# Performance work log

Hardware: AMD Instinct MI355X
Metric: run time of the kernel (lower is better)

Reference implementation:

```python
import jax, jax.numpy as jnp
import numpy as np

N = 100000   # nodes
E = 1600000  # edges
IN, H1, H2, OUT = 128, 256, 128, 16


def setup_inputs() -> dict:
    key = jax.random.key(0)
    ks = jax.random.split(key, 20)

    def lin(kw, fan_in, fan_out):
        s = 1.0 / np.sqrt(fan_in)
        return jax.random.uniform(kw, (fan_in, fan_out), jnp.float32, -s, s)

    inp = {
        "x": jax.random.normal(ks[0], (N, IN), jnp.float32),
        "edge_index": jax.random.randint(ks[1], (2, E), 0, N, jnp.int64),
        # main branch
        "W1": lin(ks[2], IN, H1), "b1": jnp.zeros((H1,), jnp.float32),
        "W2": lin(ks[3], H1, H2), "b2": jnp.zeros((H2,), jnp.float32),
        "Wc": lin(ks[4], H2, OUT), "bc": jnp.zeros((OUT,), jnp.float32),
        # encoder branch (4 GCN layers)
        "We1": lin(ks[5], IN, H2), "be1": jnp.zeros((H2,), jnp.float32),
        "We2": lin(ks[6], H2, H2), "be2": jnp.zeros((H2,), jnp.float32),
        "We3": lin(ks[7], H2, H2), "be3": jnp.zeros((H2,), jnp.float32),
        "We4": lin(ks[8], H2, H2), "be4": jnp.zeros((H2,), jnp.float32),
        # trustworthiness head
        "Wt": lin(ks[9], H2, 2), "bt": jnp.zeros((2,), jnp.float32),
    }
    return inp


def _gcn(x, W, b, row, col, dis):
    # PyG GCNConv: out = D^-1/2 (A + I) D^-1/2 (x W) + b
    xw = x @ W                                   # [N, F]
    norm = dis[row] * dis[col]                   # [E]
    msg = xw[row] * norm[:, None]                # [E, F]  (gather + scale)
    agg = jax.ops.segment_sum(msg, col, num_segments=N)
    agg = agg + xw * (dis * dis)[:, None]        # self-loop contribution
    return agg + b


def reference(x, edge_index, W1, b1, W2, b2, Wc, bc,
              We1, be1, We2, be2, We3, be3, We4, be4, Wt, bt):
    row, col = edge_index[0], edge_index[1]
    # degree with self-loops, shared across all conv layers (same graph)
    deg = jax.ops.segment_sum(jnp.ones((E,), x.dtype), col, num_segments=N) + 1.0
    dis = deg ** -0.5

    # classification branch
    h = jax.nn.relu(_gcn(x, W1, b1, row, col, dis))
    h = _gcn(h, W2, b2, row, col, dis)
    class_logits = h @ Wc + bc

    # encoder branch -> trust head
    h2 = _gcn(x, We1, be1, row, col, dis)
    h2 = _gcn(h2, We2, be2, row, col, dis)
    h2 = _gcn(h2, We3, be3, row, col, dis)
    h2 = _gcn(h2, We4, be4, row, col, dis)
    trust_prob = jax.nn.sigmoid(h2 @ Wt + bt)

    return (class_logits, trust_prob)
```

## Files before the change

### kernel.cpp

```cpp
#include <hip/hip_runtime.h>
#include <math.h>


#define SM_W2C   0
#define SM_T4    4096
#define SM_T3    4352
#define SM_T2    4608
#define SM_ME    4864
#define SM_CLSC  5120
#define SM_C1    5136
#define SM_C2    5138
#define SM_C3    5140
#define SM_FC    5142
#define SM_TOTAL 5248

typedef __attribute__((ext_vector_type(8))) short bf16x8;
typedef __attribute__((ext_vector_type(4))) float f32x4;
#define MFMA16(a, b, c) __builtin_amdgcn_mfma_f32_16x16x32_bf16(a, b, c, 0, 0, 0)

__device__ inline unsigned short f2bf(float f) {
  unsigned u = __float_as_uint(f);
  u += 0x7fffu + ((u >> 16) & 1u);
  return (unsigned short)(u >> 16);
}
__device__ inline float bf2f(unsigned short h) {
  return __uint_as_float((unsigned)h << 16);
}

__global__ __launch_bounds__(256) void k_deg(const int* __restrict__ ei,
                                             int* __restrict__ deg, int E, int N) {
  int e = blockIdx.x * 256 + threadIdx.x;
  if (e < E) {
    unsigned c = (unsigned)ei[E + e];
    if (c >= (unsigned)N) c = 0;
    atomicAdd(&deg[c], 1);
  }
}

__global__ __launch_bounds__(1024) void k_scan1(const int* __restrict__ deg,
                                                int* __restrict__ rowptr,
                                                int* __restrict__ bsum,
                                                float* __restrict__ dis,
                                                int* __restrict__ cnt, int n) {
  __shared__ int wsum[16];
  int tid = threadIdx.x, lane = tid & 63, wid = tid >> 6;
  int i = blockIdx.x * 1024 + tid;
  int v = (i < n) ? deg[i] : 0;
  if (i < n) {
    dis[i] = 1.0f / sqrtf((float)v + 1.0f);
    cnt[i] = 0;
  }
  int x = v;
  #pragma unroll
  for (int off = 1; off < 64; off <<= 1) {
    int t = __shfl_up(x, off, 64);
    if (lane >= off) x += t;
  }
  if (lane == 63) wsum[wid] = x;
  __syncthreads();
  if (wid == 0 && lane < 16) {
    int ws = wsum[lane];
    #pragma unroll
    for (int off = 1; off < 16; off <<= 1) {
      int t = __shfl_up(ws, off, 64);
      if (lane >= off) ws += t;
    }
    wsum[lane] = ws;
  }
  __syncthreads();
  int incl = x + (wid ? wsum[wid - 1] : 0);
  if (i < n) rowptr[i + 1] = incl;
  if (tid == 0) bsum[blockIdx.x] = wsum[15];
}

__global__ __launch_bounds__(128) void k_scan2(int* __restrict__ bsum,
                                               int* __restrict__ rowptr, int B) {
  __shared__ int s[128];
  int tid = threadIdx.x;
  s[tid] = (tid < B) ? bsum[tid] : 0;
  __syncthreads();
  if (tid == 0) {
    int acc = 0;
    for (int j = 0; j < B; ++j) { int t = s[j]; s[j] = acc; acc += t; }
    rowptr[0] = 0;
  }
  __syncthreads();
  if (tid < B) bsum[tid] = s[tid];
}

__global__ __launch_bounds__(256) void k_scan3(int* __restrict__ rowptr,
                                               const int* __restrict__ bsum, int n) {
  int i = blockIdx.x * 256 + threadIdx.x;
  if (i < n) rowptr[i + 1] += bsum[i >> 10];
}

__global__ __launch_bounds__(256) void k_scatter(const int* __restrict__ ei,
                                                 const int* __restrict__ rowptr,
                                                 int* __restrict__ cnt,
                                                 int* __restrict__ csr_src,
                                                 int E, int N) {
  int e = blockIdx.x * 256 + threadIdx.x;
  if (e >= E) return;
  unsigned r = (unsigned)ei[e];
  unsigned c = (unsigned)ei[E + e];
  if (r >= (unsigned)N) r = 0;
  if (c >= (unsigned)N) c = 0;
  int pos = rowptr[c] + atomicAdd(&cnt[c], 1);
  csr_src[pos] = (int)r;
}

__global__ __launch_bounds__(256) void k_precompute(
    const float* __restrict__ W1,
    const float* __restrict__ W2, const float* __restrict__ b2,
    const float* __restrict__ Wc, const float* __restrict__ bc,
    const float* __restrict__ We1, const float* __restrict__ be1,
    const float* __restrict__ We2, const float* __restrict__ be2,
    const float* __restrict__ We3, const float* __restrict__ be3,
    const float* __restrict__ We4, const float* __restrict__ be4,
    const float* __restrict__ Wt, const float* __restrict__ bt,
    float* __restrict__ sm,
    unsigned short* __restrict__ w1h, unsigned short* __restrict__ w1l,
    unsigned short* __restrict__ w2h, unsigned short* __restrict__ w2l) {
  int tid = threadIdx.x, b = blockIdx.x;
  if (b < 16) {
    int r = b * 16 + (tid >> 4), c = tid & 15;
    float s = 0.f;
    #pragma unroll 4
    for (int k = 0; k < 128; ++k) s += W2[(size_t)r * 128 + k] * Wc[k * 16 + c];
    sm[SM_W2C + r * 16 + c] = s;
    unsigned short h = f2bf(s);
    w2h[c * 256 + r] = h;
    w2l[c * 256 + r] = f2bf(s - bf2f(h));
    return;
  }
  if (b < 32) {
    int base = (b - 16) * 2048;
    #pragma unroll
    for (int it = 0; it < 8; ++it) {
      int idx = base + it * 256 + tid;
      int c = idx >> 7, k = idx & 127;
      float v = W1[(size_t)k * 256 + c];
      unsigned short h = f2bf(v);
      w1h[idx] = h;
      w1l[idx] = f2bf(v - bf2f(h));
    }
    return;
  }
  {
    int r = tid >> 1, c = tid & 1; float s = 0.f;
    for (int k = 0; k < 128; ++k) s += We4[r * 128 + k] * Wt[k * 2 + c];
    sm[SM_T4 + r * 2 + c] = s;
  }
  __syncthreads();
  {
    int r = tid >> 1, c = tid & 1; float s = 0.f;
    for (int k = 0; k < 128; ++k) s += We3[r * 128 + k] * sm[SM_T4 + k * 2 + c];
    sm[SM_T3 + r * 2 + c] = s;
  }
  __syncthreads();
  {
    int r = tid >> 1, c = tid & 1; float s = 0.f;
    for (int k = 0; k < 128; ++k) s += We2[r * 128 + k] * sm[SM_T3 + k * 2 + c];
    sm[SM_T2 + r * 2 + c] = s;
  }
  __syncthreads();
  {
    int r = tid >> 1, c = tid & 1; float s = 0.f;
    for (int k = 0; k < 128; ++k) s += We1[r * 128 + k] * sm[SM_T2 + k * 2 + c];
    sm[SM_ME + r * 2 + c] = s;
  }
  if (tid < 16) {
    float s = 0.f;
    for (int k = 0; k < 128; ++k) s += b2[k] * Wc[k * 16 + tid];
    sm[SM_CLSC + tid] = s + bc[tid];
  }
  __syncthreads();
  if (tid < 2) {
    float s = 0.f;
    for (int k = 0; k < 128; ++k) s += be1[k] * sm[SM_T2 + k * 2 + tid];
    sm[SM_C1 + tid] = s;
    s = 0.f;
    for (int k = 0; k < 128; ++k) s += be2[k] * sm[SM_T3 + k * 2 + tid];
    sm[SM_C2 + tid] = s;
    s = 0.f;
    for (int k = 0; k < 128; ++k) s += be3[k] * sm[SM_T4 + k * 2 + tid];
    sm[SM_C3 + tid] = s;
    s = 0.f;
    for (int k = 0; k < 128; ++k) s += be4[k] * Wt[k * 2 + tid];
    sm[SM_FC + tid] = s + bt[tid];
  }
}

__global__ __launch_bounds__(256) void k_agg128(
    const float* __restrict__ x, const int* __restrict__ rowptr,
    const int* __restrict__ csr_src, const float* __restrict__ dis,
    const float* __restrict__ sm,
    unsigned short* __restrict__ axh, unsigned short* __restrict__ axl,
    float* __restrict__ ga, int N) {
  int node = blockIdx.x * 4 + (threadIdx.x >> 6);
  if (node >= N) return;
  int lane = threadIdx.x & 63;
  const float2* x2 = (const float2*)x;
  float d = dis[node];
  float2 v = x2[(size_t)node * 64 + lane];
  float a0 = d * v.x, a1 = d * v.y;
  int e = rowptr[node], end = rowptr[node + 1];
  while (e < end) {
    int rem = end - e;
    int cnt = rem < 64 ? rem : 64;
    int off = lane < cnt ? lane : cnt - 1;
    int src_l = csr_src[e + off];
    int wbits = __float_as_int(dis[src_l]);
    for (int i = 0; i < cnt; ++i) {
      int s = __builtin_amdgcn_readlane(src_l, i);
      float w = __int_as_float(__builtin_amdgcn_readlane(wbits, i));
      float2 u = x2[(size_t)s * 64 + lane];
      a0 = fmaf(w, u.x, a0);
      a1 = fmaf(w, u.y, a1);
    }
    e += 64;
  }
  a0 *= d; a1 *= d;
  unsigned short h0 = f2bf(a0), h1v = f2bf(a1);
  unsigned short l0 = f2bf(a0 - bf2f(h0)), l1 = f2bf(a1 - bf2f(h1v));
  ((unsigned int*)axh)[(size_t)node * 64 + lane] = (unsigned)h0 | ((unsigned)h1v << 16);
  ((unsigned int*)axl)[(size_t)node * 64 + lane] = (unsigned)l0 | ((unsigned)l1 << 16);
  float4 me = *(const float4*)&sm[SM_ME + lane * 4];
  float p0 = a0 * me.x + a1 * me.z;
  float p1 = a0 * me.y + a1 * me.w;
  #pragma unroll
  for (int m = 32; m; m >>= 1) { p0 += __shfl_xor(p0, m); p1 += __shfl_xor(p1, m); }
  if (lane == 0)
    ((float2*)ga)[node] = make_float2(p0 + sm[SM_C1 + 0], p1 + sm[SM_C1 + 1]);
}

__global__ __launch_bounds__(256, 2) void k_gemm_mfma(
    const unsigned short* __restrict__ axh, const unsigned short* __restrict__ axl,
    const unsigned short* __restrict__ w1h, const unsigned short* __restrict__ w1l,
    const unsigned short* __restrict__ w2h, const unsigned short* __restrict__ w2l,
    const float* __restrict__ b1, float* __restrict__ Y, int N) {
  __shared__ unsigned short lds[32768];
  int tid = threadIdx.x, lane = tid & 63, w = tid >> 6;
  int r16 = lane & 15, kh = lane >> 4;
  int m0 = blockIdx.x * 64;
  #pragma unroll
  for (int it = 0; it < 8; ++it) {
    int idx = it * 256 + tid;
    int arr = idx >> 10, rem = idx & 1023;
    int row = rem >> 4, ch = rem & 15;
    int gr = m0 + row; if (gr > N - 1) gr = N - 1;
    const unsigned short* src = (arr ? axl : axh) + (size_t)gr * 128 + ch * 8;
    uint4 vv = *(const uint4*)src;
    *(uint4*)&lds[arr * 8192 + row * 128 + ((ch ^ (row & 7)) * 8)] = vv;
  }
  __syncthreads();
  f32x4 acc[4][4];
  #pragma unroll
  for (int i = 0; i < 4; ++i)
    #pragma unroll
    for (int j = 0; j < 4; ++j) acc[i][j] = (f32x4){0.f, 0.f, 0.f, 0.f};
  #pragma unroll
  for (int ks = 0; ks < 4; ++ks) {
    bf16x8 bh[4], bl[4];
    #pragma unroll
    for (int nt = 0; nt < 4; ++nt) {
      int col = w * 64 + nt * 16 + r16;
      size_t boff = (size_t)col * 128 + ks * 32 + kh * 8;
      bh[nt] = *(const bf16x8*)(w1h + boff);
      bl[nt] = *(const bf16x8*)(w1l + boff);
    }
    #pragma unroll
    for (int mt = 0; mt < 4; ++mt) {
      int row = mt * 16 + r16;
      int ch = ks * 4 + kh;
      int off = row * 128 + ((ch ^ (row & 7)) * 8);
      bf16x8 ah = *(const bf16x8*)&lds[off];
      bf16x8 al = *(const bf16x8*)&lds[8192 + off];
      #pragma unroll
      for (int nt = 0; nt < 4; ++nt) {
        acc[mt][nt] = MFMA16(ah, bh[nt], acc[mt][nt]);
        acc[mt][nt] = MFMA16(ah, bl[nt], acc[mt][nt]);
        acc[mt][nt] = MFMA16(al, bh[nt], acc[mt][nt]);
      }
    }
  }
  __syncthreads();
  #pragma unroll
  for (int nt = 0; nt < 4; ++nt) {
    int colL = w * 64 + nt * 16 + r16;
    float bv = b1[colL];
    #pragma unroll
    for (int mt = 0; mt < 4; ++mt) {
      #pragma unroll
      for (int r = 0; r < 4; ++r) {
        int rowL = mt * 16 + kh * 4 + r;
        float vv = acc[mt][nt][r] + bv;
        vv = vv > 0.f ? vv : 0.f;
        unsigned short hh = f2bf(vv);
        unsigned short ll = f2bf(vv - bf2f(hh));
        int idx = rowL * 256 + (colL ^ ((rowL & 7) << 3));
        lds[idx] = hh;
        lds[16384 + idx] = ll;
      }
    }
  }
  __syncthreads();
  f32x4 y = (f32x4){0.f, 0.f, 0.f, 0.f};
  int rowL = w * 16 + r16;
  #pragma unroll
  for (int k2 = 0; k2 < 8; ++k2) {
    int cb = k2 * 32 + kh * 8;
    int idx = rowL * 256 + (cb ^ ((rowL & 7) << 3));
    bf16x8 a2h = *(const bf16x8*)&lds[idx];
    bf16x8 a2l = *(const bf16x8*)&lds[16384 + idx];
    size_t boff = (size_t)r16 * 256 + cb;
    bf16x8 b2h = *(const bf16x8*)(w2h + boff);
    bf16x8 b2l = *(const bf16x8*)(w2l + boff);
    y = MFMA16(a2h, b2h, y);
    y = MFMA16(a2h, b2l, y);
    y = MFMA16(a2l, b2h, y);
  }
  #pragma unroll
  for (int r = 0; r < 4; ++r) {
    int gr = m0 + w * 16 + kh * 4 + r;
    if (gr < N) Y[(size_t)gr * 16 + r16] = y[r];
  }
}

__global__ __launch_bounds__(256) void k_agg18(
    const float* __restrict__ Y, const float* __restrict__ g,
    const int* __restrict__ rowptr, const int* __restrict__ csr_src,
    const float* __restrict__ dis, const float* __restrict__ sm,
    float* __restrict__ out, float* __restrict__ gout, int N) {
  int node = blockIdx.x * 16 + (threadIdx.x >> 4);
  if (node >= N) return;
  int sl = threadIdx.x & 15;
  const float2* g2 = (const float2*)g;
  float d = dis[node];
  float acc = d * Y[(size_t)node * 16 + sl];
  float2 gv = g2[node];
  float ga0 = d * gv.x, ga1 = d * gv.y;
  int e = rowptr[node], end = rowptr[node + 1];
  for (; e < end; ++e) {
    int s = csr_src[e];
    float w = dis[s];
    acc = fmaf(w, Y[(size_t)s * 16 + sl], acc);
    float2 gu = g2[s];
    ga0 = fmaf(w, gu.x, ga0);
    ga1 = fmaf(w, gu.y, ga1);
  }
  out[(size_t)node * 16 + sl] = d * acc + sm[SM_CLSC + sl];
  if (sl == 0)
    ((float2*)gout)[node] =
        make_float2(d * ga0 + sm[SM_C2 + 0], d * ga1 + sm[SM_C2 + 1]);
}

template <int FINAL>
__global__ __launch_bounds__(256) void k_agg2(
    const float* __restrict__ gin, const int* __restrict__ rowptr,
    const int* __restrict__ csr_src, const float* __restrict__ dis,
    const float* __restrict__ cadd, float* __restrict__ gout, int N) {
  int i = blockIdx.x * 256 + threadIdx.x;
  if (i >= N) return;
  const float2* g2 = (const float2*)gin;
  float d = dis[i];
  float2 v = g2[i];
  float a0 = d * v.x, a1 = d * v.y;
  int e = rowptr[i], end = rowptr[i + 1];
  for (; e < end; ++e) {
    int s = csr_src[e];
    float w = dis[s];
    float2 u = g2[s];
    a0 = fmaf(w, u.x, a0); a1 = fmaf(w, u.y, a1);
  }
  a0 = d * a0 + cadd[0]; a1 = d * a1 + cadd[1];
  if (FINAL) {
    a0 = 1.f / (1.f + expf(-a0));
    a1 = 1.f / (1.f + expf(-a1));
  }
  ((float2*)gout)[i] = make_float2(a0, a1);
}

extern "C" void kernel_launch(void* const* d_in, const int* in_sizes, int n_in,
                              void* d_out, int out_size, void* d_ws, size_t ws_size,
                              hipStream_t stream) {
  const float* x = (const float*)d_in[0];
  const int* ei = (const int*)d_in[1];
  const float* W1 = (const float*)d_in[2];
  const float* b1 = (const float*)d_in[3];
  const float* W2 = (const float*)d_in[4];
  const float* b2 = (const float*)d_in[5];
  const float* Wc = (const float*)d_in[6];
  const float* bc = (const float*)d_in[7];
  const float* We1 = (const float*)d_in[8];
  const float* be1 = (const float*)d_in[9];
  const float* We2 = (const float*)d_in[10];
  const float* be2 = (const float*)d_in[11];
  const float* We3 = (const float*)d_in[12];
  const float* be3 = (const float*)d_in[13];
  const float* We4 = (const float*)d_in[14];
  const float* be4 = (const float*)d_in[15];
  const float* Wt = (const float*)d_in[16];
  const float* bt = (const float*)d_in[17];
  float* out = (float*)d_out;

  const int N = in_sizes[0] / 128;
  const int E = in_sizes[1] / 2;
  const int NB = (N + 1023) / 1024;

  char* ws = (char*)d_ws;
  size_t off = 0;
  auto alloc = [&](size_t bytes) {
    size_t o = off;
    off = (off + bytes + 255) & ~(size_t)255;
    return o;
  };
  int* deg = (int*)(ws + alloc((size_t)N * 4));
  int* cnt = (int*)(ws + alloc((size_t)N * 4));
  int* rowptr = (int*)(ws + alloc(((size_t)N + 1) * 4));
  int* bsum = (int*)(ws + alloc(128 * 4));
  float* dis = (float*)(ws + alloc((size_t)N * 4));
  int* csr_src = (int*)(ws + alloc((size_t)E * 4));
  unsigned short* axh = (unsigned short*)(ws + alloc((size_t)N * 128 * 2));
  unsigned short* axl = (unsigned short*)(ws + alloc((size_t)N * 128 * 2));
  float* y16 = (float*)(ws + alloc((size_t)N * 16 * 4));
  float* ga = (float*)(ws + alloc((size_t)N * 2 * 4));
  float* gb = (float*)(ws + alloc((size_t)N * 2 * 4));
  float* sm = (float*)(ws + alloc((size_t)SM_TOTAL * 4));
  unsigned short* w1h = (unsigned short*)(ws + alloc(32768 * 2));
  unsigned short* w1l = (unsigned short*)(ws + alloc(32768 * 2));
  unsigned short* w2h = (unsigned short*)(ws + alloc(4096 * 2));
  unsigned short* w2l = (unsigned short*)(ws + alloc(4096 * 2));

  hipMemsetAsync(deg, 0, (size_t)N * 4, stream);

  k_precompute<<<33, 256, 0, stream>>>(W1, W2, b2, Wc, bc, We1, be1, We2, be2,
                                       We3, be3, We4, be4, Wt, bt, sm,
                                       w1h, w1l, w2h, w2l);
  k_deg<<<(E + 255) / 256, 256, 0, stream>>>(ei, deg, E, N);
  k_scan1<<<NB, 1024, 0, stream>>>(deg, rowptr, bsum, dis, cnt, N);
  k_scan2<<<1, 128, 0, stream>>>(bsum, rowptr, NB);
  k_scan3<<<(N + 255) / 256, 256, 0, stream>>>(rowptr, bsum, N);
  k_scatter<<<(E + 255) / 256, 256, 0, stream>>>(ei, rowptr, cnt, csr_src, E, N);
  k_agg128<<<(N + 3) / 4, 256, 0, stream>>>(x, rowptr, csr_src, dis, sm,
                                            axh, axl, ga, N);
  k_gemm_mfma<<<(N + 63) / 64, 256, 0, stream>>>(axh, axl, w1h, w1l, w2h, w2l,
                                                 b1, y16, N);
  k_agg18<<<(N + 15) / 16, 256, 0, stream>>>(y16, ga, rowptr, csr_src, dis, sm,
                                             out, gb, N);
  k_agg2<0><<<(N + 255) / 256, 256, 0, stream>>>(gb, rowptr, csr_src, dis,
                                                 sm + SM_C3, ga, N);
  k_agg2<1><<<(N + 255) / 256, 256, 0, stream>>>(
      ga, rowptr, csr_src, dis, sm + SM_FC, out + (size_t)N * 16, N);
}
```

Before: 601.0 us.

## Gather fp16 copy of x in first aggregation and split edges across lanes

Converts x to a packed fp16 copy inside extra blocks of the precompute kernel, so the 128-wide neighbour gather reads half the bytes per edge. The small aggregation kernels (agg18, agg2) now split each node's edge list across 4 or 8 lane groups and combine the partial sums with shuffles, to expose more memory-level parallelism. This adds a full pass over x to write the fp16 copy, and fp16 rounding of the inputs lowers accuracy.

```diff
diff --git a/kernel.cpp b/kernel.cpp
--- a/kernel.cpp
+++ b/kernel.cpp
@@ -1,4 +1,5 @@
 #include <hip/hip_runtime.h>
+#include <hip/hip_fp16.h>
 #include <math.h>
 
 
@@ -110,6 +111,7 @@
 }
 
 __global__ __launch_bounds__(256) void k_precompute(
+    const float* __restrict__ x, unsigned* __restrict__ xh, int NP4,
     const float* __restrict__ W1,
     const float* __restrict__ W2, const float* __restrict__ b2,
     const float* __restrict__ Wc, const float* __restrict__ bc,
@@ -120,8 +122,26 @@
     const float* __restrict__ Wt, const float* __restrict__ bt,
     float* __restrict__ sm,
     unsigned short* __restrict__ w1h, unsigned short* __restrict__ w1l,
-    unsigned short* __restrict__ w2h, unsigned short* __restrict__ w2l) {
+    unsigned short* __restrict__ w2h, unsigned short* __restrict__ w2l,
+    int nblk) {
   int tid = threadIdx.x, b = blockIdx.x;
+  if (b >= 33) {
+    const float4* xf4 = (const float4*)x;
+    uint4* xh4 = (uint4*)xh;
+    int nthreads = (nblk - 33) * 256;
+    for (int c = (b - 33) * 256 + tid; c < NP4; c += nthreads) {
+      float4 a = xf4[2 * c], d = xf4[2 * c + 1];
+      __half2 h0 = __floats2half2_rn(a.x, a.y);
+      __half2 h1 = __floats2half2_rn(a.z, a.w);
+      __half2 h2 = __floats2half2_rn(d.x, d.y);
+      __half2 h3 = __floats2half2_rn(d.z, d.w);
+      uint4 o;
+      o.x = *(unsigned*)&h0; o.y = *(unsigned*)&h1;
+      o.z = *(unsigned*)&h2; o.w = *(unsigned*)&h3;
+      xh4[c] = o;
+    }
+    return;
+  }
   if (b < 16) {
     int r = b * 16 + (tid >> 4), c = tid & 15;
     float s = 0.f;
@@ -192,7 +212,7 @@
 }
 
 __global__ __launch_bounds__(256) void k_agg128(
-    const float* __restrict__ x, const int* __restrict__ rowptr,
+    const unsigned* __restrict__ xh, const int* __restrict__ rowptr,
     const int* __restrict__ csr_src, const float* __restrict__ dis,
     const float* __restrict__ sm,
     unsigned short* __restrict__ axh, unsigned short* __restrict__ axl,
@@ -200,10 +220,10 @@
   int node = blockIdx.x * 4 + (threadIdx.x >> 6);
   if (node >= N) return;
   int lane = threadIdx.x & 63;
-  const float2* x2 = (const float2*)x;
   float d = dis[node];
-  float2 v = x2[(size_t)node * 64 + lane];
-  float a0 = d * v.x, a1 = d * v.y;
+  unsigned su = xh[(size_t)node * 64 + lane];
+  float2 sv = __half22float2(*(__half2*)&su);
+  float a0 = d * sv.x, a1 = d * sv.y;
   int e = rowptr[node], end = rowptr[node + 1];
   while (e < end) {
     int rem = end - e;
@@ -214,9 +234,10 @@
     for (int i = 0; i < cnt; ++i) {
       int s = __builtin_amdgcn_readlane(src_l, i);
       float w = __int_as_float(__builtin_amdgcn_readlane(wbits, i));
-      float2 u = x2[(size_t)s * 64 + lane];
-      a0 = fmaf(w, u.x, a0);
-      a1 = fmaf(w, u.y, a1);
+      unsigned u = xh[(size_t)s * 64 + lane];
+      float2 uf = __half22float2(*(__half2*)&u);
+      a0 = fmaf(w, uf.x, a0);
+      a1 = fmaf(w, uf.y, a1);
     }
     e += 64;
   }
@@ -332,16 +353,20 @@
     const int* __restrict__ rowptr, const int* __restrict__ csr_src,
     const float* __restrict__ dis, const float* __restrict__ sm,
     float* __restrict__ out, float* __restrict__ gout, int N) {
-  int node = blockIdx.x * 16 + (threadIdx.x >> 4);
+  int node = blockIdx.x * 4 + (threadIdx.x >> 6);
   if (node >= N) return;
-  int sl = threadIdx.x & 15;
+  int lane = threadIdx.x & 63;
+  int eo = lane >> 4, sl = lane & 15;
   const float2* g2 = (const float2*)g;
   float d = dis[node];
-  float acc = d * Y[(size_t)node * 16 + sl];
-  float2 gv = g2[node];
-  float ga0 = d * gv.x, ga1 = d * gv.y;
-  int e = rowptr[node], end = rowptr[node + 1];
-  for (; e < end; ++e) {
+  float acc = 0.f, ga0 = 0.f, ga1 = 0.f;
+  if (eo == 0) {
+    acc = d * Y[(size_t)node * 16 + sl];
+    float2 gv = g2[node];
+    ga0 = d * gv.x; ga1 = d * gv.y;
+  }
+  int end = rowptr[node + 1];
+  for (int e = rowptr[node] + eo; e < end; e += 4) {
     int s = csr_src[e];
     float w = dis[s];
     acc = fmaf(w, Y[(size_t)s * 16 + sl], acc);
@@ -349,8 +374,11 @@
     ga0 = fmaf(w, gu.x, ga0);
     ga1 = fmaf(w, gu.y, ga1);
   }
-  out[(size_t)node * 16 + sl] = d * acc + sm[SM_CLSC + sl];
-  if (sl == 0)
+  acc += __shfl_xor(acc, 16); acc += __shfl_xor(acc, 32);
+  ga0 += __shfl_xor(ga0, 16); ga0 += __shfl_xor(ga0, 32);
+  ga1 += __shfl_xor(ga1, 16); ga1 += __shfl_xor(ga1, 32);
+  if (lane < 16) out[(size_t)node * 16 + sl] = d * acc + sm[SM_CLSC + sl];
+  if (lane == 0)
     ((float2*)gout)[node] =
         make_float2(d * ga0 + sm[SM_C2 + 0], d * ga1 + sm[SM_C2 + 1]);
 }
@@ -360,25 +388,35 @@
     const float* __restrict__ gin, const int* __restrict__ rowptr,
     const int* __restrict__ csr_src, const float* __restrict__ dis,
     const float* __restrict__ cadd, float* __restrict__ gout, int N) {
-  int i = blockIdx.x * 256 + threadIdx.x;
+  int i = blockIdx.x * 32 + (threadIdx.x >> 3);
   if (i >= N) return;
+  int el = threadIdx.x & 7;
   const float2* g2 = (const float2*)gin;
   float d = dis[i];
-  float2 v = g2[i];
-  float a0 = d * v.x, a1 = d * v.y;
-  int e = rowptr[i], end = rowptr[i + 1];
-  for (; e < end; ++e) {
+  float a0 = 0.f, a1 = 0.f;
+  if (el == 0) {
+    float2 v = g2[i];
+    a0 = d * v.x; a1 = d * v.y;
+  }
+  int end = rowptr[i + 1];
+  for (int e = rowptr[i] + el; e < end; e += 8) {
     int s = csr_src[e];
     float w = dis[s];
     float2 u = g2[s];
     a0 = fmaf(w, u.x, a0); a1 = fmaf(w, u.y, a1);
   }
-  a0 = d * a0 + cadd[0]; a1 = d * a1 + cadd[1];
-  if (FINAL) {
-    a0 = 1.f / (1.f + expf(-a0));
-    a1 = 1.f / (1.f + expf(-a1));
-  }
-  ((float2*)gout)[i] = make_float2(a0, a1);
+  #pragma unroll
+  for (int m = 1; m < 8; m <<= 1) {
+    a0 += __shfl_xor(a0, m); a1 += __shfl_xor(a1, m);
+  }
+  if (el == 0) {
+    a0 = d * a0 + cadd[0]; a1 = d * a1 + cadd[1];
+    if (FINAL) {
+      a0 = 1.f / (1.f + expf(-a0));
+      a1 = 1.f / (1.f + expf(-a1));
+    }
+    ((float2*)gout)[i] = make_float2(a0, a1);
+  }
 }
 
 extern "C" void kernel_launch(void* const* d_in, const int* in_sizes, int n_in,
@@ -407,6 +445,8 @@
   const int N = in_sizes[0] / 128;
   const int E = in_sizes[1] / 2;
   const int NB = (N + 1023) / 1024;
+  const int NP4 = N * 128 / 8;
+  const int CVB = 1600;
 
   char* ws = (char*)d_ws;
   size_t off = 0;
@@ -421,6 +461,7 @@
   int* bsum = (int*)(ws + alloc(128 * 4));
   float* dis = (float*)(ws + alloc((size_t)N * 4));
   int* csr_src = (int*)(ws + alloc((size_t)E * 4));
+  unsigned* xh = (unsigned*)(ws + alloc((size_t)N * 128 * 2));
   unsigned short* axh = (unsigned short*)(ws + alloc((size_t)N * 128 * 2));
   unsigned short* axl = (unsigned short*)(ws + alloc((size_t)N * 128 * 2));
   float* y16 = (float*)(ws + alloc((size_t)N * 16 * 4));
@@ -434,22 +475,22 @@
 
   hipMemsetAsync(deg, 0, (size_t)N * 4, stream);
 
-  k_precompute<<<33, 256, 0, stream>>>(W1, W2, b2, Wc, bc, We1, be1, We2, be2,
-                                       We3, be3, We4, be4, Wt, bt, sm,
-                                       w1h, w1l, w2h, w2l);
+  k_precompute<<<33 + CVB, 256, 0, stream>>>(
+      x, xh, NP4, W1, W2, b2, Wc, bc, We1, be1, We2, be2, We3, be3, We4, be4,
+      Wt, bt, sm, w1h, w1l, w2h, w2l, 33 + CVB);
   k_deg<<<(E + 255) / 256, 256, 0, stream>>>(ei, deg, E, N);
   k_scan1<<<NB, 1024, 0, stream>>>(deg, rowptr, bsum, dis, cnt, N);
   k_scan2<<<1, 128, 0, stream>>>(bsum, rowptr, NB);
   k_scan3<<<(N + 255) / 256, 256, 0, stream>>>(rowptr, bsum, N);
   k_scatter<<<(E + 255) / 256, 256, 0, stream>>>(ei, rowptr, cnt, csr_src, E, N);
-  k_agg128<<<(N + 3) / 4, 256, 0, stream>>>(x, rowptr, csr_src, dis, sm,
+  k_agg128<<<(N + 3) / 4, 256, 0, stream>>>(xh, rowptr, csr_src, dis, sm,
                                             axh, axl, ga, N);
   k_gemm_mfma<<<(N + 63) / 64, 256, 0, stream>>>(axh, axl, w1h, w1l, w2h, w2l,
                                                  b1, y16, N);
-  k_agg18<<<(N + 15) / 16, 256, 0, stream>>>(y16, ga, rowptr, csr_src, dis, sm,
-                                             out, gb, N);
-  k_agg2<0><<<(N + 255) / 256, 256, 0, stream>>>(gb, rowptr, csr_src, dis,
-                                                 sm + SM_C3, ga, N);
-  k_agg2<1><<<(N + 255) / 256, 256, 0, stream>>>(
+  k_agg18<<<(N + 3) / 4, 256, 0, stream>>>(y16, ga, rowptr, csr_src, dis, sm,
+                                           out, gb, N);
+  k_agg2<0><<<(N + 31) / 32, 256, 0, stream>>>(gb, rowptr, csr_src, dis,
+                                               sm + SM_C3, ga, N);
+  k_agg2<1><<<(N + 31) / 32, 256, 0, stream>>>(
       ga, rowptr, csr_src, dis, sm + SM_FC, out + (size_t)N * 16, N);
 }
```

Measured after the change: 581.4 us. -3.3%, faster.
